# Performance work log

Measured on AMD Instinct MI355X. Metric: run time of the kernel, lower is better.

Reference implementation:

```python
import jax, jax.numpy as jnp
import numpy as np
from jax import lax

B, T1, T2, D, H = 4, 1024, 1024, 1024, 16
DK = D // H          # 64 per-head dim
K = 13               # conv kernel size
FF = 4 * D


def _ln(x, g, b, eps):
    mu = jnp.mean(x, axis=-1, keepdims=True)
    var = jnp.mean((x - mu) ** 2, axis=-1, keepdims=True)
    y = (x - mu) * lax.rsqrt(var + eps)
    if g is not None:
        y = y * g + b
    return y


def _conv1d(x, w, b):
    # x: (B, T, C) ; w: (O, C//H, K) grouped conv, 'same' padding
    y = lax.conv_general_dilated(
        x.transpose(0, 2, 1), w, window_strides=(1,),
        padding=[(K // 2, K // 2)],
        dimension_numbers=('NCH', 'OIH', 'NCH'),
        feature_group_count=H)
    return (y + b[None, :, None]).transpose(0, 2, 1)


def setup_inputs() -> dict:
    key = jax.random.key(0)
    ks = jax.random.split(key, 24)
    s = 0.02
    inp = {
        'noisy_feats': jax.random.normal(ks[0], (B, T1, D), jnp.float32),
        'clean_feats': jax.random.normal(ks[1], (B, T2, D), jnp.float32),
        't': jax.random.normal(ks[2], (B, D), jnp.float32),
        'ln_noisy_g': jnp.ones((D,), jnp.float32),
        'ln_noisy_b': jnp.zeros((D,), jnp.float32),
        'ln_clean_g': jnp.ones((D,), jnp.float32),
        'ln_clean_b': jnp.zeros((D,), jnp.float32),
        'ada_w': jax.random.normal(ks[3], (6 * D, D), jnp.float32) * s,
        'ada_b': jnp.zeros((6 * D,), jnp.float32),
        'wq': jax.random.normal(ks[4], (D, D // H, K), jnp.float32) * s,
        'bq': jnp.zeros((D,), jnp.float32),
        'wk': jax.random.normal(ks[5], (D, D // H, K), jnp.float32) * s,
        'bk': jnp.zeros((D,), jnp.float32),
        'wv': jax.random.normal(ks[6], (D, D // H, K), jnp.float32) * s,
        'bv': jnp.zeros((D,), jnp.float32),
        'fc_w': jax.random.normal(ks[7], (D, D), jnp.float32) * s,
        'fc_b': jnp.zeros((D,), jnp.float32),
        'ff_w1': jax.random.normal(ks[8], (FF, D), jnp.float32) * s,
        'ff_b1': jnp.zeros((FF,), jnp.float32),
        'ff_w2': jax.random.normal(ks[9], (D, FF), jnp.float32) * s,
        'ff_b2': jnp.zeros((D,), jnp.float32),
        'noisy_lengths': jax.random.randint(ks[10], (B,), 1, T1 + 1),
        'clean_lengths': jax.random.randint(ks[11], (B,), 1, T2 + 1),
    }
    return inp


def reference(noisy_feats, clean_feats, t,
              ln_noisy_g, ln_noisy_b, ln_clean_g, ln_clean_b,
              ada_w, ada_b, wq, bq, wk, bk, wv, bv, fc_w, fc_b,
              ff_w1, ff_b1, ff_w2, ff_b2,
              noisy_lengths, clean_lengths):
    # pre-norms (affine, eps=1e-5 torch default)
    noisy = _ln(noisy_feats, ln_noisy_g, ln_noisy_b, 1e-5)
    clean = _ln(clean_feats, ln_clean_g, ln_clean_b, 1e-5)

    # AdaLayerNormZero
    emb = jax.nn.silu(t) @ ada_w.T + ada_b                      # (B, 6D)
    shift_msa, scale_msa, gate_msa, shift_mlp, scale_mlp, gate_mlp = jnp.split(emb, 6, axis=1)
    normx = _ln(noisy, None, None, 1e-6) * (1.0 + scale_msa[:, None]) + shift_msa[:, None]

    # padding mask: True at pad positions (only context mask enters the scores)
    clean_mask = jnp.arange(T2)[None, :] >= clean_lengths[:, None]   # (B, T2)

    # grouped-conv QKV
    q = _conv1d(normx, wq, bq).reshape(B, T1, H, DK)
    k = _conv1d(clean, wk, bk).reshape(B, T2, H, DK)
    v = _conv1d(clean, wv, bv).reshape(B, T2, H, DK)

    scores = jnp.einsum('bqhd,bkhd->bhqk', q, k) / jnp.sqrt(jnp.float32(DK))
    scores = jnp.where(clean_mask[:, None, None, :], jnp.float32(-1e30), scores)
    p = jax.nn.softmax(scores, axis=-1)
    # rows where every key is masked -> zero (torch all_inf handling)
    all_masked = jnp.all(clean_mask, axis=-1)[:, None, None, None]
    p = jnp.where(all_masked, 0.0, p)

    out = jnp.einsum('bhqk,bkhd->bqhd', p, v).reshape(B, T1, D)
    out = out @ fc_w.T + fc_b

    x = noisy + gate_msa[:, None, :] * out
    n2 = _ln(x, None, None, 1e-6) * (1.0 + scale_mlp[:, None]) + shift_mlp[:, None]
    ff = jax.nn.gelu(n2 @ ff_w1.T + ff_b1, approximate=True) @ ff_w2.T + ff_b2
    return x + gate_mlp[:, None, :] * ff
```

## Files before the change

kernel.cpp:

```cpp
#include <hip/hip_runtime.h>
#include <hip/hip_bf16.h>

typedef __hip_bfloat16 bf16;
typedef __attribute__((ext_vector_type(8))) short short8;
typedef __attribute__((ext_vector_type(4))) float f32x4;

#define D_ 1024
#define SIXD 6144

__device__ __forceinline__ float bflo(unsigned int u){ union {unsigned int u; float f;} c; c.u = u << 16; return c.f; }
__device__ __forceinline__ float bfhi(unsigned int u){ union {unsigned int u; float f;} c; c.u = u & 0xFFFF0000u; return c.f; }
__device__ __forceinline__ float bload(const bf16* p){
  union {unsigned int u; float f;} c;
  c.u = ((unsigned int)(*reinterpret_cast<const unsigned short*>(p))) << 16;
  return c.f;
}
__device__ __forceinline__ bf16 bstore(float f){ return __float2bfloat16(f); }
__device__ __forceinline__ unsigned short bf16bits(float f){
  bf16 b = __float2bfloat16(f);
  return *reinterpret_cast<unsigned short*>(&b);
}

__device__ __forceinline__ void gload16(const bf16* g, bf16* l){
  __builtin_amdgcn_global_load_lds((const __attribute__((address_space(1))) unsigned int*)g,
                                   (__attribute__((address_space(3))) unsigned int*)l, 16, 0, 0);
}

template<int ISBF>
__device__ __forceinline__ float ild(const void* p, size_t i){
  if (ISBF) return bload((const bf16*)p + i);
  return ((const float*)p)[i];
}

__device__ __forceinline__ float block_sum(float v, float* sh4){
  #pragma unroll
  for (int o = 32; o; o >>= 1) v += __shfl_down(v, o);
  __syncthreads();
  int lane = threadIdx.x & 63, wid = threadIdx.x >> 6;
  if (lane == 0) sh4[wid] = v;
  __syncthreads();
  return sh4[0] + sh4[1] + sh4[2] + sh4[3];
}

__global__ void detect_kernel(const unsigned int* g, int* flag){
  unsigned int u = *g;
  *flag = (u == 0x3F803F80u) ? 1 : 0;
}

template<int ISBF>
__device__ __forceinline__ void emb_body(const void* T, const void* AW, const void* AB,
                                         float* E, float* st){
  int b = blockIdx.y;
  int tid = threadIdx.x;
  for (int c = tid; c < D_; c += 256) {
    float x = ild<ISBF>(T, (size_t)b*D_ + c);
    st[c] = x / (1.f + expf(-x));
  }
  __syncthreads();
  int wid = tid >> 6, lane = tid & 63;
  int j = blockIdx.x * 4 + wid;
  float dot = 0.f;
  for (int c = lane; c < D_; c += 64) dot += ild<ISBF>(AW, (size_t)j*D_ + c) * st[c];
  #pragma unroll
  for (int o = 32; o; o >>= 1) dot += __shfl_down(dot, o);
  if (lane == 0) E[b*SIXD + j] = dot + ild<ISBF>(AB, j);
}
__global__ __launch_bounds__(256) void emb_kernel(const void* T, const void* AW, const void* AB,
                                                  const int* flagp, float* E){
  __shared__ float st[D_];
  if (*flagp) emb_body<1>(T, AW, AB, E, st); else emb_body<0>(T, AW, AB, E, st);
}

template<int ISBF>
__device__ __forceinline__ void ln_noisy_body(const void* X, const void* G, const void* Bt,
                                              const float* E, bf16* xbuf, bf16* normx, float* sh4){
  int r = blockIdx.x; int b = r >> 10;
  int tid = threadIdx.x; int c0 = tid * 4;
  size_t base = (size_t)r*D_ + c0;
  float f0 = ild<ISBF>(X, base+0), f1 = ild<ISBF>(X, base+1);
  float f2 = ild<ISBF>(X, base+2), f3 = ild<ISBF>(X, base+3);
  float mean = block_sum(f0+f1+f2+f3, sh4) * (1.f/D_);
  float var  = block_sum(f0*f0+f1*f1+f2*f2+f3*f3, sh4) * (1.f/D_) - mean*mean;
  float rstd = rsqrtf(fmaxf(var, 0.f) + 1e-5f);
  float y0 = (f0-mean)*rstd*ild<ISBF>(G,c0+0) + ild<ISBF>(Bt,c0+0);
  float y1 = (f1-mean)*rstd*ild<ISBF>(G,c0+1) + ild<ISBF>(Bt,c0+1);
  float y2 = (f2-mean)*rstd*ild<ISBF>(G,c0+2) + ild<ISBF>(Bt,c0+2);
  float y3 = (f3-mean)*rstd*ild<ISBF>(G,c0+3) + ild<ISBF>(Bt,c0+3);
  bf16* xo = xbuf + base;
  xo[0]=bstore(y0); xo[1]=bstore(y1); xo[2]=bstore(y2); xo[3]=bstore(y3);
  float m2 = block_sum(y0+y1+y2+y3, sh4) * (1.f/D_);
  float v2 = block_sum(y0*y0+y1*y1+y2*y2+y3*y3, sh4) * (1.f/D_) - m2*m2;
  float rstd2 = rsqrtf(fmaxf(v2, 0.f) + 1e-6f);
  const float* eb = E + b*SIXD;
  bf16* o = normx + base;
  o[0] = bstore((y0-m2)*rstd2*(1.f+eb[1024+c0+0]) + eb[c0+0]);
  o[1] = bstore((y1-m2)*rstd2*(1.f+eb[1024+c0+1]) + eb[c0+1]);
  o[2] = bstore((y2-m2)*rstd2*(1.f+eb[1024+c0+2]) + eb[c0+2]);
  o[3] = bstore((y3-m2)*rstd2*(1.f+eb[1024+c0+3]) + eb[c0+3]);
}
__global__ __launch_bounds__(256) void ln_noisy_fused(const void* X, const void* G, const void* Bt,
                                                      const float* E, bf16* xbuf, bf16* normx,
                                                      const int* flagp){
  __shared__ float sh4[4];
  if (*flagp) ln_noisy_body<1>(X,G,Bt,E,xbuf,normx,sh4); else ln_noisy_body<0>(X,G,Bt,E,xbuf,normx,sh4);
}

template<int ISBF>
__device__ __forceinline__ void ln_clean_body(const void* X, const void* G, const void* Bt,
                                              bf16* Y, float* sh4){
  int r = blockIdx.x;
  int tid = threadIdx.x; int c0 = tid * 4;
  size_t base = (size_t)r*D_ + c0;
  float f0 = ild<ISBF>(X, base+0), f1 = ild<ISBF>(X, base+1);
  float f2 = ild<ISBF>(X, base+2), f3 = ild<ISBF>(X, base+3);
  float mean = block_sum(f0+f1+f2+f3, sh4) * (1.f/D_);
  float var  = block_sum(f0*f0+f1*f1+f2*f2+f3*f3, sh4) * (1.f/D_) - mean*mean;
  float rstd = rsqrtf(fmaxf(var, 0.f) + 1e-5f);
  bf16* o = Y + base;
  o[0] = bstore((f0-mean)*rstd*ild<ISBF>(G,c0+0) + ild<ISBF>(Bt,c0+0));
  o[1] = bstore((f1-mean)*rstd*ild<ISBF>(G,c0+1) + ild<ISBF>(Bt,c0+1));
  o[2] = bstore((f2-mean)*rstd*ild<ISBF>(G,c0+2) + ild<ISBF>(Bt,c0+2));
  o[3] = bstore((f3-mean)*rstd*ild<ISBF>(G,c0+3) + ild<ISBF>(Bt,c0+3));
}
__global__ __launch_bounds__(256) void ln_clean_kernel(const void* X, const void* G, const void* Bt,
                                                       bf16* Y, const int* flagp){
  __shared__ float sh4[4];
  if (*flagp) ln_clean_body<1>(X,G,Bt,Y,sh4); else ln_clean_body<0>(X,G,Bt,Y,sh4);
}

__global__ __launch_bounds__(256) void ln2_kernel(const bf16* __restrict__ X, const float* __restrict__ E,
                                                  bf16* __restrict__ Y){
  __shared__ float sh4[4];
  int r = blockIdx.x; int b = r >> 10;
  int tid = threadIdx.x; int c0 = tid * 4;
  uint2 u = *reinterpret_cast<const uint2*>(X + (size_t)r*D_ + c0);
  float f0 = bflo(u.x), f1 = bfhi(u.x), f2 = bflo(u.y), f3 = bfhi(u.y);
  float mean = block_sum(f0+f1+f2+f3, sh4) * (1.f/D_);
  float var  = block_sum(f0*f0+f1*f1+f2*f2+f3*f3, sh4) * (1.f/D_) - mean*mean;
  float rstd = rsqrtf(fmaxf(var, 0.f) + 1e-6f);
  const float* eb = E + b*SIXD;
  bf16* o = Y + (size_t)r*D_ + c0;
  o[0] = bstore((f0-mean)*rstd*(1.f+eb[4096+c0+0]) + eb[3072+c0+0]);
  o[1] = bstore((f1-mean)*rstd*(1.f+eb[4096+c0+1]) + eb[3072+c0+1]);
  o[2] = bstore((f2-mean)*rstd*(1.f+eb[4096+c0+2]) + eb[3072+c0+2]);
  o[3] = bstore((f3-mean)*rstd*(1.f+eb[4096+c0+3]) + eb[3072+c0+3]);
}

template<int ISBF>
__device__ __forceinline__ void wtrans_body(const void* W, bf16* Wtr){
  size_t idx = (size_t)blockIdx.x * 256 + threadIdx.x;
  int si = idx & 63;
  size_t r = idx >> 6;
  int o = (int)(r & 63); r >>= 6;
  int k = (int)(r % 13);
  int g = (int)(r / 13);
  int i = si ^ ((o & 7) << 3);
  Wtr[idx] = bstore(ild<ISBF>(W, ((size_t)(g*64 + o)*64 + i)*13 + k));
}
__global__ __launch_bounds__(256) void conv_wtrans(const void* W, bf16* Wtr, const int* flagp){
  if (*flagp) wtrans_body<1>(W, Wtr); else wtrans_body<0>(W, Wtr);
}

template<int ISBF>
__device__ __forceinline__ void wconv_body(const void* W, bf16* o, int n){
  for (int i = blockIdx.x*256 + threadIdx.x; i < n; i += gridDim.x*256)
    o[i] = bstore(ild<ISBF>(W, (size_t)i));
}
__global__ __launch_bounds__(256) void wconv_kernel(const void* W, bf16* o, int n, const int* flagp){
  if (*flagp) wconv_body<1>(W, o, n); else wconv_body<0>(W, o, n);
}

template<int ISBF>
__device__ __forceinline__ void convl_body(const bf16* __restrict__ X,
                                           const bf16* __restrict__ Wtr, const void* Bias,
                                           bf16* __restrict__ Y,
                                           bf16* ws, bf16* xs){
  int tid = threadIdx.x;
  int wave = tid >> 6, lane = tid & 63;
  int fr = lane & 15, fq = lane >> 4;
  int t0 = blockIdx.x * 256;
  int g = blockIdx.y, b = blockIdx.z;
  const bf16* Wg = Wtr + (size_t)g*53248;
  #pragma unroll
  for (int p = 0; p < 13; ++p)
    gload16(Wg + ((size_t)p*512 + tid)*8, ws + (p*512 + tid)*8);
  const bf16* xg = X + ((size_t)b*1024)*D_ + g*64;
  for (int idx = tid; idx < 268*8; idx += 512) {
    int row = idx >> 3, q = idx & 7;
    int t = t0 - 6 + row;
    uint4 v = make_uint4(0,0,0,0);
    if (t >= 0 && t < 1024)
      v = *reinterpret_cast<const uint4*>(xg + (size_t)t*D_ + q*8);
    *reinterpret_cast<uint4*>(&xs[row*72 + q*8]) = v;
  }
  __syncthreads();
  f32x4 acc[2][4];
  #pragma unroll
  for (int i = 0; i < 2; ++i)
    #pragma unroll
    for (int j = 0; j < 4; ++j) acc[i][j] = (f32x4){0.f,0.f,0.f,0.f};
  int wrow = wave * 32;
  const bf16* a0 = xs + (wrow + fr)*72 + fq*8;
  for (int k = 0; k < 13; ++k) {
    const bf16* wk_ = ws + (k*64 + fr)*64;
    const bf16* ar = a0 + k*72;
    #pragma unroll
    for (int h = 0; h < 2; ++h) {
      int swz = (h*32 + fq*8) ^ ((fr & 7) << 3);
      short8 af0 = *reinterpret_cast<const short8*>(ar + h*32);
      short8 af1 = *reinterpret_cast<const short8*>(ar + 16*72 + h*32);
      #pragma unroll
      for (int tn = 0; tn < 4; ++tn) {
        short8 bv = *reinterpret_cast<const short8*>(wk_ + tn*1024 + swz);
        acc[0][tn] = __builtin_amdgcn_mfma_f32_16x16x32_bf16(af0, bv, acc[0][tn], 0,0,0);
        acc[1][tn] = __builtin_amdgcn_mfma_f32_16x16x32_bf16(af1, bv, acc[1][tn], 0,0,0);
      }
    }
  }
  #pragma unroll
  for (int tm = 0; tm < 2; ++tm) {
    #pragma unroll
    for (int tn = 0; tn < 4; ++tn) {
      int oc = g*64 + tn*16 + fr;
      float bb = ild<ISBF>(Bias, oc);
      #pragma unroll
      for (int r = 0; r < 4; ++r) {
        int tt = t0 + wrow + tm*16 + fq*4 + r;
        Y[((size_t)(b*1024 + tt))*D_ + oc] = bstore(acc[tm][tn][r] + bb);
      }
    }
  }
}
__global__ __launch_bounds__(512) void conv_lds(const bf16* X, const bf16* Wtr, const void* Bias,
                                                bf16* Y, const int* flagp){
  extern __shared__ bf16 smem[];
  bf16* ws = smem;
  bf16* xs = smem + 53248;
  if (*flagp) convl_body<1>(X, Wtr, Bias, Y, ws, xs);
  else        convl_body<0>(X, Wtr, Bias, Y, ws, xs);
}
#define CONV_LDS_BYTES ((53248 + 268*72) * 2)

__global__ __launch_bounds__(256) void attn_mfma(const bf16* __restrict__ Q, const bf16* __restrict__ Kb,
                                                 const bf16* __restrict__ V, const int* __restrict__ lens,
                                                 bf16* __restrict__ O){
  __shared__ bf16 qs[64*72];
  __shared__ bf16 ks[64*72];
  __shared__ bf16 vt[64*72];
  __shared__ bf16 ps[4][16*72];
  int tid = threadIdx.x;
  int wave = tid >> 6, lane = tid & 63;
  int fr = lane & 15, fq = lane >> 4;
  int qb = blockIdx.x, h = blockIdx.y, b = blockIdx.z;
  int len = lens[b]; len = len < 0 ? 0 : (len > 1024 ? 1024 : len);
  {
    int row = tid >> 2, col = (tid & 3) * 16;
    const bf16* src = Q + ((size_t)(b*1024 + qb*64 + row))*D_ + h*64 + col;
    *reinterpret_cast<uint4*>(&qs[row*72 + col])     = *reinterpret_cast<const uint4*>(src);
    *reinterpret_cast<uint4*>(&qs[row*72 + col + 8]) = *reinterpret_cast<const uint4*>(src + 8);
  }
  __syncthreads();
  short8 bq0 = *reinterpret_cast<const short8*>(&qs[(wave*16 + fr)*72 + fq*8]);
  short8 bq1 = *reinterpret_cast<const short8*>(&qs[(wave*16 + fr)*72 + 32 + fq*8]);
  f32x4 oacc[4];
  #pragma unroll
  for (int t = 0; t < 4; ++t) oacc[t] = (f32x4){0.f,0.f,0.f,0.f};
  float m_ = -1e30f, l_ = 0.f;
  int krow = tid >> 2, kcol = (tid & 3) * 16;
  int vk = (tid >> 3) * 2, vcol = (tid & 7) * 8;
  const bf16* kg = Kb + ((size_t)b*1024)*D_ + h*64;
  const bf16* vg = V  + ((size_t)b*1024)*D_ + h*64;
  for (int k0 = 0; k0 < len; k0 += 64) {
    uint4 kv0 = make_uint4(0,0,0,0), kv1 = make_uint4(0,0,0,0);
    uint4 va = make_uint4(0,0,0,0), vb = make_uint4(0,0,0,0);
    if (k0 + krow < len) {
      kv0 = *reinterpret_cast<const uint4*>(kg + (size_t)(k0+krow)*D_ + kcol);
      kv1 = *reinterpret_cast<const uint4*>(kg + (size_t)(k0+krow)*D_ + kcol + 8);
    }
    if (k0 + vk < len)     va = *reinterpret_cast<const uint4*>(vg + (size_t)(k0+vk)*D_ + vcol);
    if (k0 + vk + 1 < len) vb = *reinterpret_cast<const uint4*>(vg + (size_t)(k0+vk+1)*D_ + vcol);
    __syncthreads();
    *reinterpret_cast<uint4*>(&ks[krow*72 + kcol])     = kv0;
    *reinterpret_cast<uint4*>(&ks[krow*72 + kcol + 8]) = kv1;
    {
      union { uint4 u; unsigned short s[8]; } ca, cb; ca.u = va; cb.u = vb;
      #pragma unroll
      for (int j = 0; j < 8; ++j) {
        unsigned int w = ((unsigned int)cb.s[j] << 16) | (unsigned int)ca.s[j];
        int d = vcol + j;
        int blk = ((vk >> 3) ^ ((d >> 3) & 7)) << 3;
        *reinterpret_cast<unsigned int*>(&vt[d*72 + blk + (vk & 7)]) = w;
      }
    }
    __syncthreads();
    f32x4 s[4];
    #pragma unroll
    for (int f = 0; f < 4; ++f) {
      short8 ak0 = *reinterpret_cast<const short8*>(&ks[(f*16 + fr)*72 + fq*8]);
      short8 ak1 = *reinterpret_cast<const short8*>(&ks[(f*16 + fr)*72 + 32 + fq*8]);
      s[f] = (f32x4){0.f,0.f,0.f,0.f};
      s[f] = __builtin_amdgcn_mfma_f32_16x16x32_bf16(ak0, bq0, s[f], 0,0,0);
      s[f] = __builtin_amdgcn_mfma_f32_16x16x32_bf16(ak1, bq1, s[f], 0,0,0);
    }
    float p[4][4];
    float pmax = -1e30f;
    #pragma unroll
    for (int f = 0; f < 4; ++f)
      #pragma unroll
      for (int r = 0; r < 4; ++r) {
        float sv = (k0 + f*16 + fq*4 + r < len) ? s[f][r]*0.125f : -1e30f;
        p[f][r] = sv;
        pmax = fmaxf(pmax, sv);
      }
    pmax = fmaxf(pmax, __shfl_xor(pmax, 16));
    pmax = fmaxf(pmax, __shfl_xor(pmax, 32));
    float mnew = fmaxf(m_, pmax);
    float alpha = __expf(m_ - mnew);
    float psum = 0.f;
    #pragma unroll
    for (int f = 0; f < 4; ++f)
      #pragma unroll
      for (int r = 0; r < 4; ++r) {
        float pv = __expf(p[f][r] - mnew);
        p[f][r] = pv;
        psum += pv;
      }
    psum += __shfl_xor(psum, 16);
    psum += __shfl_xor(psum, 32);
    l_ = l_*alpha + psum;
    m_ = mnew;
    #pragma unroll
    for (int f = 0; f < 4; ++f) {
      unsigned int lo = ((unsigned int)bf16bits(p[f][1]) << 16) | (unsigned int)bf16bits(p[f][0]);
      unsigned int hi = ((unsigned int)bf16bits(p[f][3]) << 16) | (unsigned int)bf16bits(p[f][2]);
      unsigned int* pp = reinterpret_cast<unsigned int*>(&ps[wave][fr*72 + f*16 + fq*4]);
      pp[0] = lo; pp[1] = hi;
    }
    float aq[4];
    #pragma unroll
    for (int r = 0; r < 4; ++r) aq[r] = __shfl(alpha, fq*4 + r);
    #pragma unroll
    for (int tn = 0; tn < 4; ++tn)
      #pragma unroll
      for (int r = 0; r < 4; ++r) oacc[tn][r] *= aq[r];
    short8 ap0 = *reinterpret_cast<const short8*>(&ps[wave][fr*72 + fq*8]);
    short8 ap1 = *reinterpret_cast<const short8*>(&ps[wave][fr*72 + 32 + fq*8]);
    #pragma unroll
    for (int tn = 0; tn < 4; ++tn) {
      int d = tn*16 + fr;
      int sw = (d >> 3) & 7;
      short8 bv0 = *reinterpret_cast<const short8*>(&vt[d*72 + ((fq     ^ sw) << 3)]);
      short8 bv1 = *reinterpret_cast<const short8*>(&vt[d*72 + (((4+fq) ^ sw) << 3)]);
      oacc[tn] = __builtin_amdgcn_mfma_f32_16x16x32_bf16(ap0, bv0, oacc[tn], 0,0,0);
      oacc[tn] = __builtin_amdgcn_mfma_f32_16x16x32_bf16(ap1, bv1, oacc[tn], 0,0,0);
    }
  }
  float linv = (l_ > 0.f) ? 1.f/l_ : 0.f;
  float iq[4];
  #pragma unroll
  for (int r = 0; r < 4; ++r) iq[r] = __shfl(linv, fq*4 + r);
  #pragma unroll
  for (int r = 0; r < 4; ++r) {
    int q = qb*64 + wave*16 + fq*4 + r;
    bf16* op = O + ((size_t)(b*1024 + q))*D_ + h*64 + fr;
    #pragma unroll
    for (int tn = 0; tn < 4; ++tn)
      op[tn*16] = bstore(oacc[tn][r] * iq[r]);
  }
}

template<int ISBF>
__device__ __forceinline__ void mgemm_body(const bf16* __restrict__ A, const bf16* __restrict__ W,
                                           const void* bias, int bofs,
                                           int K, int ldA, int ldW, int Nst, int mode, int gate_ofs,
                                           bf16* xbuf, const float* emb, void* outb,
                                           bf16* As, bf16* Bs){
  int tid = threadIdx.x;
  int flat = blockIdx.y * gridDim.x + blockIdx.x;
  int cx = gridDim.x >> 1;
  int cy = gridDim.y >> 2;
  int xcd = flat & 7;
  int idx = flat >> 3;
  int rby = idx / cx, rbx = idx - rby*cx;
  int by = (xcd & 3)*cy + rby;
  int bx = (xcd >> 2)*cx + rbx;
  int m0 = by * 128, n0 = bx * 128;
  int wave = tid >> 6, lane = tid & 63;
  int wr = wave >> 2, wc = wave & 3;
  int fr = lane & 15, fq = lane >> 4;
  int srow = tid >> 2, skc = (tid & 3) * 8;
  const bf16* Ag = A + (size_t)(m0 + srow)*ldA + skc;
  const bf16* Wg = W + (size_t)(n0 + srow)*ldW + skc;
  bf16* Asl = As + tid*8;
  bf16* Bsl = Bs + tid*8;
  const bf16* Afr = As + (wr*64 + fr)*32 + fq*8;
  const bf16* Bfr = Bs + (wc*32 + fr)*32 + fq*8;
  f32x4 acc[4][2];
  #pragma unroll
  for (int i = 0; i < 4; ++i)
    #pragma unroll
    for (int j = 0; j < 2; ++j) acc[i][j] = (f32x4){0.f,0.f,0.f,0.f};
  int nt = K >> 6;
  gload16(Ag,       Asl);
  gload16(Ag + 32,  Asl + 4096);
  gload16(Wg,       Bsl);
  gload16(Wg + 32,  Bsl + 4096);
  gload16(Ag + 64,  Asl + 8192);
  gload16(Ag + 96,  Asl + 8192 + 4096);
  gload16(Wg + 64,  Bsl + 8192);
  gload16(Wg + 96,  Bsl + 8192 + 4096);
  int tmain = nt - 4;
  for (int t4 = 0; t4 < tmain; t4 += 4) {
    const bf16* Agt = Ag + ((t4 + 2) << 6);
    const bf16* Wgt = Wg + ((t4 + 2) << 6);
    #pragma unroll
    for (int u = 0; u < 4; ++u) {
      const int bo = ((u + 2) & 3) * 8192;
      gload16(Agt + (u << 6),      Asl + bo);
      gload16(Agt + (u << 6) + 32, Asl + bo + 4096);
      gload16(Wgt + (u << 6),      Bsl + bo);
      gload16(Wgt + (u << 6) + 32, Bsl + bo + 4096);
      asm volatile("s_waitcnt vmcnt(8)" ::: "memory");
      __builtin_amdgcn_sched_barrier(0);
      __builtin_amdgcn_s_barrier();
      __builtin_amdgcn_sched_barrier(0);
      const int co = u * 8192;
      __builtin_amdgcn_s_setprio(1);
      #pragma unroll
      for (int ks = 0; ks < 2; ++ks) {
        short8 af[4], bfv[2];
        #pragma unroll
        for (int tm = 0; tm < 4; ++tm) af[tm] = *reinterpret_cast<const short8*>(Afr + co + ks*4096 + tm*16*32);
        #pragma unroll
        for (int tn = 0; tn < 2; ++tn) bfv[tn] = *reinterpret_cast<const short8*>(Bfr + co + ks*4096 + tn*16*32);
        #pragma unroll
        for (int tm = 0; tm < 4; ++tm)
          #pragma unroll
          for (int tn = 0; tn < 2; ++tn)
            acc[tm][tn] = __builtin_amdgcn_mfma_f32_16x16x32_bf16(af[tm], bfv[tn], acc[tm][tn], 0, 0, 0);
      }
      __builtin_amdgcn_s_setprio(0);
    }
  }
  {
    const bf16* Agt = Ag + ((tmain + 2) << 6);
    const bf16* Wgt = Wg + ((tmain + 2) << 6);
    #pragma unroll
    for (int u = 0; u < 4; ++u) {
      if (u < 2) {
        const int bo = ((u + 2) & 3) * 8192;
        gload16(Agt + (u << 6),      Asl + bo);
        gload16(Agt + (u << 6) + 32, Asl + bo + 4096);
        gload16(Wgt + (u << 6),      Bsl + bo);
        gload16(Wgt + (u << 6) + 32, Bsl + bo + 4096);
        asm volatile("s_waitcnt vmcnt(8)" ::: "memory");
      } else if (u == 2) {
        asm volatile("s_waitcnt vmcnt(4)" ::: "memory");
      } else {
        asm volatile("s_waitcnt vmcnt(0)" ::: "memory");
      }
      __builtin_amdgcn_sched_barrier(0);
      __builtin_amdgcn_s_barrier();
      __builtin_amdgcn_sched_barrier(0);
      const int co = u * 8192;
      __builtin_amdgcn_s_setprio(1);
      #pragma unroll
      for (int ks = 0; ks < 2; ++ks) {
        short8 af[4], bfv[2];
        #pragma unroll
        for (int tm = 0; tm < 4; ++tm) af[tm] = *reinterpret_cast<const short8*>(Afr + co + ks*4096 + tm*16*32);
        #pragma unroll
        for (int tn = 0; tn < 2; ++tn) bfv[tn] = *reinterpret_cast<const short8*>(Bfr + co + ks*4096 + tn*16*32);
        #pragma unroll
        for (int tm = 0; tm < 4; ++tm)
          #pragma unroll
          for (int tn = 0; tn < 2; ++tn)
            acc[tm][tn] = __builtin_amdgcn_mfma_f32_16x16x32_bf16(af[tm], bfv[tn], acc[tm][tn], 0, 0, 0);
      }
      __builtin_amdgcn_s_setprio(0);
    }
  }
  #pragma unroll
  for (int tm = 0; tm < 4; ++tm) {
    #pragma unroll
    for (int tn = 0; tn < 2; ++tn) {
      int nn = n0 + wc*32 + tn*16 + fr;
      float bv = bias ? ild<ISBF>(bias, (size_t)(bofs + nn)) : 0.f;
      #pragma unroll
      for (int r = 0; r < 4; ++r) {
        int mm = m0 + wr*64 + tm*16 + fq*4 + r;
        float v = acc[tm][tn][r] + bv;
        const float* eb = emb + (mm >> 10)*SIXD;
        if (mode == 1) {
          float tt = 0.7978845608028654f * (v + 0.044715f * v * v * v);
          ((bf16*)outb)[(size_t)mm*Nst + nn] = bstore(0.5f * v * (1.f + tanhf(tt)));
        } else if (mode == 2) {
          size_t xi = (size_t)mm*1024 + nn;
          xbuf[xi] = bstore(bload(xbuf + xi) + eb[gate_ofs + nn] * v);
        } else {
          size_t xi = (size_t)mm*1024 + nn;
          float rr = bload(xbuf + xi) + eb[gate_ofs + nn] * v;
          if (ISBF) ((bf16*)outb)[xi] = bstore(rr);
          else      ((float*)outb)[xi] = rr;
        }
      }
    }
  }
}
__global__ __launch_bounds__(512) void mgemm_kernel(const bf16* A, const bf16* W,
                                                    const void* bias, int bofs,
                                                    int K, int ldA, int ldW, int Nst, int mode, int gate_ofs,
                                                    bf16* xbuf, const float* emb, void* outb,
                                                    const int* flagp){
  extern __shared__ bf16 gsm[];
  bf16* As = gsm;
  bf16* Bs = gsm + 32768;
  if (*flagp) mgemm_body<1>(A,W,bias,bofs,K,ldA,ldW,Nst,mode,gate_ofs,xbuf,emb,outb,As,Bs);
  else        mgemm_body<0>(A,W,bias,bofs,K,ldA,ldW,Nst,mode,gate_ofs,xbuf,emb,outb,As,Bs);
}
#define MGEMM_LDS_BYTES (65536 * 2)

extern "C" void kernel_launch(void* const* d_in, const int* in_sizes, int n_in,
                              void* d_out, int out_size, void* d_ws, size_t ws_size,
                              hipStream_t stream) {
  (void)in_sizes; (void)n_in; (void)out_size; (void)ws_size;
  const void* noisy = d_in[0];
  const void* clean = d_in[1];
  const void* t     = d_in[2];
  const void* lng   = d_in[3];
  const void* lnb   = d_in[4];
  const void* lcg   = d_in[5];
  const void* lcb   = d_in[6];
  const void* ada_w = d_in[7];
  const void* ada_b = d_in[8];
  const void* wq    = d_in[9];
  const void* bq    = d_in[10];
  const void* wk    = d_in[11];
  const void* bk    = d_in[12];
  const void* wv    = d_in[13];
  const void* bv    = d_in[14];
  const void* fc_w  = d_in[15];
  const void* fc_b  = d_in[16];
  const void* ff_w1 = d_in[17];
  const void* ff_b1 = d_in[18];
  const void* ff_w2 = d_in[19];
  const void* ff_b2 = d_in[20];
  const int*  clen  = (const int*)d_in[22];

  char* w = (char*)d_ws;
  int*   flagp = (int*)w;
  float* embp  = (float*)(w + 4096);
  bf16*  xbuf  = (bf16*)(w + 102400);
  bf16*  normx = (bf16*)(w + 8491008);
  bf16*  cleanb= (bf16*)(w + 16879616);
  bf16*  qb    = (bf16*)(w + 25268224);
  bf16*  kbuf  = (bf16*)(w + 33656832);
  bf16*  vbuf  = (bf16*)(w + 42045440);
  bf16*  wqtr  = (bf16*)(w + 50434048);
  bf16*  wktr  = (bf16*)(w + 52137984);
  bf16*  wvtr  = (bf16*)(w + 53841920);
  bf16*  ff1h  = qb;
  bf16*  attno = cleanb;
  bf16*  n2b   = normx;
  bf16*  fc_wb = wqtr;
  bf16*  ffw1b = vbuf;
  bf16*  ffw2b = cleanb;

  detect_kernel<<<1, 1, 0, stream>>>((const unsigned int*)lng, flagp);
  emb_kernel<<<dim3(1536, 4), 256, 0, stream>>>(t, ada_w, ada_b, flagp, embp);
  ln_noisy_fused<<<4096, 256, 0, stream>>>(noisy, lng, lnb, embp, xbuf, normx, flagp);
  ln_clean_kernel<<<4096, 256, 0, stream>>>(clean, lcg, lcb, cleanb, flagp);
  conv_wtrans<<<3328, 256, 0, stream>>>(wq, wqtr, flagp);
  conv_wtrans<<<3328, 256, 0, stream>>>(wk, wktr, flagp);
  conv_wtrans<<<3328, 256, 0, stream>>>(wv, wvtr, flagp);
  conv_lds<<<dim3(4, 16, 4), 512, CONV_LDS_BYTES, stream>>>(normx,  wqtr, bq, qb,   flagp);
  conv_lds<<<dim3(4, 16, 4), 512, CONV_LDS_BYTES, stream>>>(cleanb, wktr, bk, kbuf, flagp);
  conv_lds<<<dim3(4, 16, 4), 512, CONV_LDS_BYTES, stream>>>(cleanb, wvtr, bv, vbuf, flagp);
  wconv_kernel<<<1024, 256, 0, stream>>>(fc_w, fc_wb, 1048576, flagp);
  attn_mfma<<<dim3(16, 16, 4), 256, 0, stream>>>(qb, kbuf, vbuf, clen, attno);
  wconv_kernel<<<2048, 256, 0, stream>>>(ff_w1, ffw1b, 4194304, flagp);
  mgemm_kernel<<<dim3(8, 32), 512, MGEMM_LDS_BYTES, stream>>>(attno, fc_wb, fc_b, 0,
                                                1024, 1024, 1024, 1024, 2, 2048, xbuf, embp, nullptr, flagp);
  wconv_kernel<<<2048, 256, 0, stream>>>(ff_w2, ffw2b, 4194304, flagp);
  ln2_kernel<<<4096, 256, 0, stream>>>(xbuf, embp, n2b);
  mgemm_kernel<<<dim3(16, 32), 512, MGEMM_LDS_BYTES, stream>>>(n2b, ffw1b, ff_b1, 0,
                                                 1024, 1024, 1024, 2048, 1, 0, xbuf, embp, ff1h, flagp);
  mgemm_kernel<<<dim3(8, 32), 512, MGEMM_LDS_BYTES, stream>>>(ff1h, ffw2b, ff_b2, 0,
                                                2048, 2048, 4096, 1024, 2, 5120, xbuf, embp, nullptr, flagp);
  mgemm_kernel<<<dim3(16, 32), 512, MGEMM_LDS_BYTES, stream>>>(n2b, ffw1b + (size_t)2048*1024, ff_b1, 2048,
                                                 1024, 1024, 1024, 2048, 1, 0, xbuf, embp, ff1h, flagp);
  mgemm_kernel<<<dim3(8, 32), 512, MGEMM_LDS_BYTES, stream>>>(ff1h, ffw2b + 2048, nullptr, 0,
                                                2048, 2048, 4096, 1024, 3, 5120, xbuf, embp, d_out, flagp);
}
```

Measured before the change: 445.2 us.

## Add specialized 256x128-tile triple-buffered GEMM for FF1 with fast GELU

Adds a dedicated FF1 GEMM kernel with 256x128 output tiles, a fixed K of 1024, triple-buffered LDS loads issued directly from global memory, explicit vmcnt waits with barriers, and an XCD-aware block remapping. The larger tile is meant to raise reuse per LDS load, and the deeper pipeline is meant to hide load latency. GELU's tanh is rewritten in the equivalent sigmoid form using __expf to cut epilogue cost. The tradeoffs are more accumulator registers per thread, more LDS per block and lower occupancy, with a small precision difference from the fast exp.

```diff
diff --git a/kernel.cpp b/kernel.cpp
--- a/kernel.cpp
+++ b/kernel.cpp
@@ -21,9 +21,27 @@
   return *reinterpret_cast<unsigned short*>(&b);
 }
 
+__device__ __forceinline__ float gelu_t(float v){
+  float ar = 1.5957691216057308f * (v + 0.044715f * v * v * v);
+  return v / (1.f + __expf(-ar));
+}
+
 __device__ __forceinline__ void gload16(const bf16* g, bf16* l){
   __builtin_amdgcn_global_load_lds((const __attribute__((address_space(1))) unsigned int*)g,
                                    (__attribute__((address_space(3))) unsigned int*)l, 16, 0, 0);
+}
+
+__device__ __forceinline__ void mg_sync6(){
+  asm volatile("s_waitcnt vmcnt(6)" ::: "memory");
+  __builtin_amdgcn_sched_barrier(0);
+  __builtin_amdgcn_s_barrier();
+  __builtin_amdgcn_sched_barrier(0);
+}
+__device__ __forceinline__ void mg_sync0(){
+  asm volatile("s_waitcnt vmcnt(0)" ::: "memory");
+  __builtin_amdgcn_sched_barrier(0);
+  __builtin_amdgcn_s_barrier();
+  __builtin_amdgcn_sched_barrier(0);
 }
 
 template<int ISBF>
@@ -492,8 +510,7 @@
         float v = acc[tm][tn][r] + bv;
         const float* eb = emb + (mm >> 10)*SIXD;
         if (mode == 1) {
-          float tt = 0.7978845608028654f * (v + 0.044715f * v * v * v);
-          ((bf16*)outb)[(size_t)mm*Nst + nn] = bstore(0.5f * v * (1.f + tanhf(tt)));
+          ((bf16*)outb)[(size_t)mm*Nst + nn] = bstore(gelu_t(v));
         } else if (mode == 2) {
           size_t xi = (size_t)mm*1024 + nn;
           xbuf[xi] = bstore(bload(xbuf + xi) + eb[gate_ofs + nn] * v);
@@ -519,6 +536,95 @@
   else        mgemm_body<0>(A,W,bias,bofs,K,ldA,ldW,Nst,mode,gate_ofs,xbuf,emb,outb,As,Bs);
 }
 #define MGEMM_LDS_BYTES (65536 * 2)
+
+template<int ISBF>
+__device__ __forceinline__ void mgemm256_body(const bf16* __restrict__ A, const bf16* __restrict__ W,
+                                              const void* bias, int bofs, int Nst,
+                                              bf16* __restrict__ outb, bf16* As, bf16* Bs){
+  int tid = threadIdx.x;
+  int flat = blockIdx.y * gridDim.x + blockIdx.x;
+  int cx = gridDim.x >> 1, cy = gridDim.y >> 2;
+  int xcd = flat & 7, idx = flat >> 3;
+  int rby = idx / cx, rbx = idx - rby*cx;
+  int by = (xcd & 3)*cy + rby;
+  int bx = (xcd >> 2)*cx + rbx;
+  int m0 = by * 256, n0 = bx * 128;
+  int wave = tid >> 6, lane = tid & 63;
+  int wr = wave >> 1, wc = wave & 1;
+  int fr = lane & 15, fq = lane >> 4;
+  const bf16* Ag0 = A + (size_t)(m0 + (tid >> 2))*1024 + (tid & 3)*8;
+  const bf16* Ag1 = Ag0 + (size_t)128*1024;
+  const bf16* Wg  = W + (size_t)(n0 + (tid >> 2))*1024 + (tid & 3)*8;
+  bf16* Asl = As + tid*8;
+  bf16* Bsl = Bs + tid*8;
+  const bf16* Afr = As + (wr >> 1)*4096 + ((wr & 1)*64 + fr)*32 + fq*8;
+  const bf16* Bfr = Bs + (wc*64 + fr)*32 + fq*8;
+  f32x4 acc[4][4];
+  #pragma unroll
+  for (int i = 0; i < 4; ++i)
+    #pragma unroll
+    for (int j = 0; j < 4; ++j) acc[i][j] = (f32x4){0.f,0.f,0.f,0.f};
+  auto issue = [&](int t, int buf){
+    gload16(Ag0 + (t << 6),      Asl + buf*16384);
+    gload16(Ag0 + (t << 6) + 32, Asl + buf*16384 + 8192);
+    gload16(Ag1 + (t << 6),      Asl + buf*16384 + 4096);
+    gload16(Ag1 + (t << 6) + 32, Asl + buf*16384 + 8192 + 4096);
+    gload16(Wg  + (t << 6),      Bsl + buf*8192);
+    gload16(Wg  + (t << 6) + 32, Bsl + buf*8192 + 4096);
+  };
+  auto comp = [&](int buf){
+    __builtin_amdgcn_s_setprio(1);
+    #pragma unroll
+    for (int ks = 0; ks < 2; ++ks) {
+      short8 af[4], bfv[4];
+      #pragma unroll
+      for (int tm = 0; tm < 4; ++tm) af[tm] = *reinterpret_cast<const short8*>(Afr + buf*16384 + ks*8192 + tm*512);
+      #pragma unroll
+      for (int tn = 0; tn < 4; ++tn) bfv[tn] = *reinterpret_cast<const short8*>(Bfr + buf*8192 + ks*4096 + tn*512);
+      #pragma unroll
+      for (int tm = 0; tm < 4; ++tm)
+        #pragma unroll
+        for (int tn = 0; tn < 4; ++tn)
+          acc[tm][tn] = __builtin_amdgcn_mfma_f32_16x16x32_bf16(af[tm], bfv[tn], acc[tm][tn], 0, 0, 0);
+    }
+    __builtin_amdgcn_s_setprio(0);
+  };
+  issue(0, 0);
+  issue(1, 1);
+  #pragma unroll
+  for (int g = 0; g < 4; ++g) {
+    mg_sync6(); issue(3*g + 2, 2); comp(0);
+    mg_sync6(); issue(3*g + 3, 0); comp(1);
+    mg_sync6(); issue(3*g + 4, 1); comp(2);
+  }
+  mg_sync6(); issue(14, 2); comp(0);
+  mg_sync6(); issue(15, 0); comp(1);
+  mg_sync6();               comp(2);
+  mg_sync0();               comp(0);
+  #pragma unroll
+  for (int tm = 0; tm < 4; ++tm) {
+    #pragma unroll
+    for (int tn = 0; tn < 4; ++tn) {
+      int nn = n0 + wc*64 + tn*16 + fr;
+      float bv = ild<ISBF>(bias, (size_t)(bofs + nn));
+      #pragma unroll
+      for (int r = 0; r < 4; ++r) {
+        int mm = m0 + wr*64 + tm*16 + fq*4 + r;
+        outb[(size_t)mm*Nst + nn] = bstore(gelu_t(acc[tm][tn][r] + bv));
+      }
+    }
+  }
+}
+__global__ __launch_bounds__(512) void mgemm256_kernel(const bf16* A, const bf16* W,
+                                                       const void* bias, int bofs, int Nst,
+                                                       bf16* outb, const int* flagp){
+  extern __shared__ bf16 gsm[];
+  bf16* As = gsm;
+  bf16* Bs = gsm + 49152;
+  if (*flagp) mgemm256_body<1>(A, W, bias, bofs, Nst, outb, As, Bs);
+  else        mgemm256_body<0>(A, W, bias, bofs, Nst, outb, As, Bs);
+}
+#define MG256_LDS_BYTES ((49152 + 24576) * 2)
 
 extern "C" void kernel_launch(void* const* d_in, const int* in_sizes, int n_in,
                               void* d_out, int out_size, void* d_ws, size_t ws_size,
@@ -583,12 +689,12 @@
                                                 1024, 1024, 1024, 1024, 2, 2048, xbuf, embp, nullptr, flagp);
   wconv_kernel<<<2048, 256, 0, stream>>>(ff_w2, ffw2b, 4194304, flagp);
   ln2_kernel<<<4096, 256, 0, stream>>>(xbuf, embp, n2b);
-  mgemm_kernel<<<dim3(16, 32), 512, MGEMM_LDS_BYTES, stream>>>(n2b, ffw1b, ff_b1, 0,
-                                                 1024, 1024, 1024, 2048, 1, 0, xbuf, embp, ff1h, flagp);
+  mgemm256_kernel<<<dim3(16, 16), 512, MG256_LDS_BYTES, stream>>>(n2b, ffw1b, ff_b1, 0,
+                                                                  2048, ff1h, flagp);
   mgemm_kernel<<<dim3(8, 32), 512, MGEMM_LDS_BYTES, stream>>>(ff1h, ffw2b, ff_b2, 0,
                                                 2048, 2048, 4096, 1024, 2, 5120, xbuf, embp, nullptr, flagp);
-  mgemm_kernel<<<dim3(16, 32), 512, MGEMM_LDS_BYTES, stream>>>(n2b, ffw1b + (size_t)2048*1024, ff_b1, 2048,
-                                                 1024, 1024, 1024, 2048, 1, 0, xbuf, embp, ff1h, flagp);
+  mgemm256_kernel<<<dim3(16, 16), 512, MG256_LDS_BYTES, stream>>>(n2b, ffw1b + (size_t)2048*1024, ff_b1, 2048,
+                                                                  2048, ff1h, flagp);
   mgemm_kernel<<<dim3(8, 32), 512, MGEMM_LDS_BYTES, stream>>>(ff1h, ffw2b + 2048, nullptr, 0,
                                                 2048, 2048, 4096, 1024, 3, 5120, xbuf, embp, d_out, flagp);
 }
```

Result: faster. 427.1 us (-4.1%).
